# Kernel tuning notes

Hardware: AMD Instinct MI355X
Metric: run time of the kernel (lower is better)

The kernel has to match this reference:

```python
import jax, jax.numpy as jnp
from jax import lax
import numpy as np

SHEET = 160; AFF_K = 15; AFF_C = 2; AFF_DIL = 1
LAT_K = 25; LAT_DIL = 2; LAT_ITERS = 10
EXC_RANGE = 5.0
HOMEO_TARGET = 0.02
FLOAT_MULT = 0.1
INH_EXC_BAL = 0.55
STRENGTH = 1.0


def _dist(size):
    c = (size - 1) / 2.0
    a = np.arange(size) - c
    return np.sqrt(a[:, None] ** 2 + a[None, :] ** 2)


def get_circle(size, radius):
    return (_dist(size) < radius).astype(np.float32)


def get_radial_cos(size, radius):
    return np.cos(np.clip(_dist(size) / radius, 0.0, 1.0) * (np.pi / 2)).astype(np.float32)


def _constants():
    env = get_radial_cos(AFF_K, AFF_K) ** 2 * get_circle(AFF_K, AFF_K / 2)
    env = env / env.max()
    aff_env = np.tile(env[None, None], (1, AFF_C, 1, 1)).reshape(1, -1, 1)
    e = int(round(EXC_RANGE)); e = e if e % 2 == 1 else e + 1  # oddenise
    sre = get_radial_cos(e, EXC_RANGE) ** 2 * get_circle(e, e / 2)
    sre = sre / sre.sum()
    inh_mask = get_radial_cos(LAT_K, e / LAT_DIL) ** 2 * get_circle(LAT_K, e / (2 * LAT_DIL))
    lri = get_radial_cos(LAT_K, LAT_K) ** 2 * get_circle(LAT_K, LAT_K / 2) * (1.0 - inh_mask)
    lri = lri.reshape(1, -1, 1); lri = lri / lri.max()
    return jnp.asarray(aff_env), jnp.asarray(sre)[None, None], jnp.asarray(lri), e


def _unfold(x, k, dil):
    # F.unfold equivalent: (N, C*k*k, L), channel-major (c, kh, kw) ordering
    p = lax.conv_general_dilated_patches(x, (k, k), (1, 1), 'VALID', rhs_dilation=(dil, dil))
    n, f, h, w = p.shape
    return p.reshape(n, f, h * w)


def setup_inputs():
    key = jax.random.key(0)
    k1, k2, k3 = jax.random.split(key, 3)
    in_hw = SHEET + AFF_K - 1
    x = jax.random.uniform(k1, (1, AFF_C, in_hw, in_hw), dtype=jnp.float32)
    rfs = jax.random.uniform(k2, (SHEET * SHEET, AFF_C * AFF_K * AFF_K, 1), dtype=jnp.float32) + 0.1
    lat_weights = jax.random.uniform(k3, (SHEET * SHEET, LAT_K * LAT_K, 1), dtype=jnp.float32) + 0.1
    adathresh = jnp.zeros((1, 1, SHEET, SHEET), jnp.float32)
    return {"x": x, "rfs": rfs, "lat_weights": lat_weights, "adathresh": adathresh}


def _forward(x, rfs, lat_weights, adathresh):
    aff_env, sre, lri, e = _constants()
    sg = lax.stop_gradient
    F_aff = rfs.shape[1]; F_lat = lat_weights.shape[1]
    # no-grad in-place weight renormalisation
    rfs_n = rfs / sg(rfs.sum(1, keepdims=True) / (F_aff * FLOAT_MULT))
    latw_n = lat_weights / sg(lat_weights.sum(1, keepdims=True) / (F_lat * FLOAT_MULT))
    lat_w = sg(latw_n) / (F_lat * FLOAT_MULT)  # detached lateral weights
    # afferent locally-connected (unshared) receptive fields: unfold + per-location dot
    x_tiles = _unfold(x, AFF_K, AFF_DIL) * aff_env          # (1, F_aff, L)
    x_tiles = jnp.transpose(x_tiles, (2, 0, 1))             # (L, 1, F_aff)
    raw_aff = jnp.einsum('lof,lfo->l', x_tiles, rfs_n).reshape(1, 1, SHEET, SHEET)
    aff = sg(raw_aff) / (F_aff * FLOAT_MULT) - adathresh
    lat = jax.nn.relu(aff)
    pos_pad = e // 2
    pad = (LAT_K // 2) * LAT_DIL
    lat_mean0 = jnp.zeros_like(lat)

    def body(carry, _):
        l, lm = carry
        l = jnp.pad(l, ((0, 0), (0, 0), (pos_pad, pos_pad), (pos_pad, pos_pad)), constant_values=HOMEO_TARGET)
        l = lax.conv_general_dilated(l, sre, (1, 1), 'VALID', dimension_numbers=('NCHW', 'OIHW', 'NCHW'))
        lp = jnp.pad(l, ((0, 0), (0, 0), (pad, pad), (pad, pad)), constant_values=HOMEO_TARGET)
        tiles = _unfold(lp, LAT_K, LAT_DIL) * lri           # (1, F_lat, L)
        tiles = jnp.transpose(tiles, (2, 0, 1))             # (L, 1, F_lat)
        lat_neg = jnp.einsum('lof,lfo->l', tiles, lat_w).reshape(1, 1, SHEET, SHEET)
        l = l * (1.0 - INH_EXC_BAL) - lat_neg * INH_EXC_BAL
        l = l * STRENGTH + aff
        l = jnp.tanh(jax.nn.relu(l))
        return (l, lm + l), None

    (lat, lat_mean), _ = lax.scan(body, (lat, lat_mean0), None, length=LAT_ITERS)
    lat_mean = sg(lat_mean / LAT_ITERS)
    # hebbian lateral correlation term (grad flows to lat_weights only)
    lmp = jnp.pad(lat_mean, ((0, 0), (0, 0), (pad, pad), (pad, pad)), constant_values=HOMEO_TARGET)
    tiles = _unfold(lmp, LAT_K, LAT_DIL) * lri              # (1, F_lat, L)
    tiles = jnp.transpose(tiles, (2, 0, 1)) * lat_mean.reshape(SHEET * SHEET, 1, 1)
    lat_correlations = jnp.einsum('lof,lfo->', tiles, latw_n)
    return raw_aff, lat, lat_correlations


def reference(x, rfs, lat_weights, adathresh):
    return _forward(x, rfs, lat_weights, adathresh)
```

## Files before the change

kernel.cpp:

```cpp
#include <hip/hip_runtime.h>
#include <math.h>

#define SHEET 160
#define LTOT (SHEET*SHEET)
#define F_AFF 450
#define F_LAT 625
#define N_ITERS 10
#define IN_HW 174
#define HOMEO 0.02f
#define PI_D 3.14159265358979323846

typedef float f32x4 __attribute__((ext_vector_type(4)));

#define BH 10
#define BW 10
#define BLK 640
#define TCOLS (SHEET/BW)
#define GRID_L ((SHEET/BH)*TCOLS)
#define EH 58
#define EWH 30
#define EP_HALF (EH*EWH)
#define EP_N (2*EP_HALF)
#define LW 64
#define LH 62
#define LT_N (LH*LW)

#define PBLK 256
#define RPB 8
#define NABLK (LTOT/RPB)

#define NPAIR 256

#define WS_SRE    0
#define WS_PKF    32
#define WS_PKL    544
#define WS_OFFT   1056
#define WS_AFFTAB 1568
#define WS_AFF    2592
#define WS_B0     (WS_AFF + LTOT)
#define WS_B1     (WS_B0  + LTOT)
#define WS_LM     (WS_B1  + LTOT)
#define WS_WQ     (WS_LM  + LTOT + 64)

__device__ __forceinline__ float wred_dpp(float v) {
    v += __int_as_float(__builtin_amdgcn_update_dpp(0, __float_as_int(v), 0x111, 0xf, 0xf, true));
    v += __int_as_float(__builtin_amdgcn_update_dpp(0, __float_as_int(v), 0x112, 0xf, 0xf, true));
    v += __int_as_float(__builtin_amdgcn_update_dpp(0, __float_as_int(v), 0x114, 0xf, 0xf, true));
    v += __int_as_float(__builtin_amdgcn_update_dpp(0, __float_as_int(v), 0x118, 0xf, 0xf, true));
    v += __int_as_float(__builtin_amdgcn_update_dpp(0, __float_as_int(v), 0x142, 0xa, 0xf, true));
    v += __int_as_float(__builtin_amdgcn_update_dpp(0, __float_as_int(v), 0x143, 0xc, 0xf, true));
    return v;
}

__device__ __forceinline__ unsigned f2bf(float f) {
    unsigned u = __float_as_uint(f);
    return (u + 0x7FFFu + ((u >> 16) & 1u)) >> 16;
}

__global__ __launch_bounds__(1024) void k_init(float* __restrict__ ws,
                                               float* __restrict__ out) {
    __shared__ float red[1024];
    __shared__ float lriS[640];
    __shared__ int   nzf[512];
    __shared__ int   wcnt[16];
    const int t = threadIdx.x;
    const int lane = t & 63, wvi = t >> 6;

    if (t == 0) out[2 * LTOT] = 0.f;

    float sre_raw = 0.f;
    if (t < 25) {
        int u = t / 5, v = t % 5;
        double d = sqrt((double)((u-2)*(u-2) + (v-2)*(v-2)));
        if (d < 2.5) { double cv = cos(fmin(d/5.0, 1.0) * PI_D * 0.5); sre_raw = (float)(cv*cv); }
    }

    float lri_raw = 0.f;
    const int dy = t / 25, dx = t % 25;
    if (t < 625) {
        double d = sqrt((double)((dy-12)*(dy-12) + (dx-12)*(dx-12)));
        double base = 0.0, inh = 0.0;
        if (d < 12.5) { double cv = cos(fmin(d/25.0, 1.0) * PI_D * 0.5); base = cv*cv; }
        if (d < 1.25) { double cv = cos(fmin(d/2.5,  1.0) * PI_D * 0.5); inh  = cv*cv; }
        lri_raw = (float)(base * (1.0 - inh));
    }
    const bool nz = (lri_raw != 0.f);
    if (t < 640) lriS[t] = lri_raw;

    red[t] = lri_raw;
    __syncthreads();
    #pragma unroll
    for (int s = 512; s > 0; s >>= 1) {
        if (t < s) red[t] = fmaxf(red[t], red[t + s]);
        __syncthreads();
    }
    const float lri_max = red[0];
    __syncthreads();

    red[t] = sre_raw;
    __syncthreads();
    #pragma unroll
    for (int s = 512; s > 0; s >>= 1) {
        if (t < s) red[t] += red[t + s];
        __syncthreads();
    }
    const float sre_sum = red[0];

    if (t < 32) ws[WS_SRE + t] = (t < 25) ? sre_raw / sre_sum : 0.f;

    unsigned long long bal = __ballot(nz);
    if (lane == 0) wcnt[wvi] = __popcll(bal);
    __syncthreads();
    int woff = 0, ntot = 0;
    #pragma unroll
    for (int v2 = 0; v2 < 16; ++v2) { int c = wcnt[v2]; if (v2 < wvi) woff += c; ntot += c; }
    if (nz) nzf[woff + __popcll(bal & ((1ull << lane) - 1ull))] = t;
    __syncthreads();

    if (t < 256) {
        #pragma unroll
        for (int h = 0; h < 2; ++h) {
            int idx = 2*t + h;
            int f = 624, off = 0; float lv = 0.f;
            if (idx < ntot) {
                f = nzf[idx];
                int fy = f / 25, fx = f - 25*fy;
                off = fy * (2*EWH) + fx;
                lv = lriS[f] / lri_max;
            }
            int slot = (2*(t >> 6) + h)*64 + (t & 63);
            ((int*)  (ws + WS_PKF ))[slot] = f;
            ((float*)(ws + WS_PKL ))[slot] = lv;
            ((int*)  (ws + WS_OFFT))[slot] = off;
        }
    }

    if (t < 512) {
        float ev = 0.f; int off = 0;
        if (t < 450) {
            int c  = t / 225, rr = t % 225;
            int kh = rr / 15, kw = rr % 15;
            double d = sqrt((double)((kh-7)*(kh-7) + (kw-7)*(kw-7)));
            if (d < 7.5) { double cv = cos(fmin(d/15.0, 1.0) * PI_D * 0.5); ev = (float)(cv*cv); }
            off = c * (IN_HW*IN_HW) + kh * IN_HW + kw;
        }
        ((float2*)(ws + WS_AFFTAB))[t] = make_float2(ev, __int_as_float(off));
    }
}

__global__ __launch_bounds__(PBLK, 8) void k_pre(const float* __restrict__ x,
                                                 const float* __restrict__ rfs,
                                                 const float* __restrict__ latw,
                                                 const float* __restrict__ ada,
                                                 float* __restrict__ out_rawaff,
                                                 float* __restrict__ ws,
                                                 unsigned* __restrict__ wq) {
    __shared__ __align__(16) float S[5008];
    const int tid = threadIdx.x;
    const int w = tid >> 6, lane = tid & 63;

    if (blockIdx.x < NABLK) {
        const int l0 = blockIdx.x * RPB;
        const f32x4* src4 = (const f32x4*)(rfs + (size_t)l0 * F_AFF);
        #pragma unroll
        for (int k = 0; k < 4; ++k) {
            int idx = k * PBLK + tid;
            if (idx < 900) ((f32x4*)S)[idx] = __builtin_nontemporal_load(src4 + idx);
        }

        float envA[8]; int offA[8];
        const float2* atab = (const float2*)(ws + WS_AFFTAB);
        #pragma unroll
        for (int it = 0; it < 8; ++it) {
            float2 tb = atab[it*64 + lane];
            envA[it] = tb.x; offA[it] = __float_as_int(tb.y);
        }
        __syncthreads();

        #pragma unroll
        for (int s = 0; s < 2; ++s) {
            const int row = 2*w + s, l = l0 + row;
            const int i = l / SHEET, j = l % SHEET;
            const int xbase = i * IN_HW + j;
            const float* Srow = S + row * F_AFF;
            float dot = 0.f, rs = 0.f;
            #pragma unroll
            for (int it = 0; it < 8; ++it) {
                int f = it*64 + lane;
                float r = (f < F_AFF) ? Srow[f] : 0.f;
                float xv = x[xbase + offA[it]];
                dot = fmaf(xv * envA[it], r, dot);
                rs += r;
            }
            dot = wred_dpp(dot); rs = wred_dpp(rs);
            if (lane == 63) {
                float a = dot / rs;
                out_rawaff[l] = 45.0f * a;
                float aff = a - ada[l];
                ws[WS_AFF + l] = aff;
                ws[WS_B0  + l] = fmaxf(aff, 0.f);
                ws[WS_LM  + l] = 0.f;
            }
        }
    } else {
        const int l0 = (blockIdx.x - NABLK) * RPB;
        const f32x4* src4 = (const f32x4*)(latw + (size_t)l0 * F_LAT);
        #pragma unroll
        for (int k = 0; k < 5; ++k) {
            int idx = k * PBLK + tid;
            if (idx < 1250) ((f32x4*)S)[idx] = __builtin_nontemporal_load(src4 + idx);
        }

        int pf[8]; float pl[8];
        #pragma unroll
        for (int q8 = 0; q8 < 8; ++q8) {
            pf[q8] = ((const int*)  (ws + WS_PKF))[q8*64 + lane];
            pl[q8] = ((const float*)(ws + WS_PKL))[q8*64 + lane];
        }
        __syncthreads();

        #pragma unroll
        for (int s = 0; s < 2; ++s) {
            const int row = 2*w + s, l = l0 + row;
            const float* Srow = S + row * F_LAT;
            float sum = 0.f;
            #pragma unroll
            for (int it = 0; it < 10; ++it) {
                int f = it*64 + lane;
                sum += (f < F_LAT) ? Srow[f] : 0.f;
            }
            sum = wred_dpp(sum);
            const float inv = 1.0f / __int_as_float(__builtin_amdgcn_readlane(__float_as_int(sum), 63));
            unsigned* dst = wq + (size_t)l * NPAIR;
            #pragma unroll
            for (int q = 0; q < 4; ++q) {
                unsigned lo = f2bf(Srow[pf[2*q]]     * pl[2*q]     * inv);
                unsigned hi = f2bf(Srow[pf[2*q + 1]] * pl[2*q + 1] * inv);
                dst[q*64 + lane] = lo | (hi << 16);
            }
        }
    }
}

__global__ __launch_bounds__(BLK, 3) void k_lat(const unsigned* __restrict__ wq,
                                                float* __restrict__ ws,
                                                const float* __restrict__ lsrc,
                                                float* __restrict__ lat_out) {
    __shared__ float Lt[LT_N];
    __shared__ float Ep[EP_N];
    const int b  = blockIdx.x;
    const int i0 = (b / TCOLS) * BH;
    const int j0 = (b % TCOLS) * BW;
    const int tid = threadIdx.x;
    const int w = tid >> 6, lane = tid & 63;
    const int lrow = (i0 + w) * SHEET + j0;

    const int* offT = (const int*)(ws + WS_OFFT);
    int offr[8];
    #pragma unroll
    for (int q8 = 0; q8 < 8; ++q8) offr[q8] = offT[q8*64 + lane];

    unsigned wp[10][4];
    #pragma unroll
    for (int s = 0; s < 10; ++s) {
        const unsigned* row = wq + (size_t)(lrow + s) * NPAIR;
        #pragma unroll
        for (int k = 0; k < 4; ++k) wp[s][k] = row[k*64 + lane];
    }
    __builtin_amdgcn_sched_barrier(0);

    float sreg[25];
    #pragma unroll
    for (int q = 0; q < 25; ++q) sreg[q] = ws[WS_SRE + q];

    for (int idx = tid; idx < LT_N; idx += BLK) {
        int r = idx >> 6, c = idx & 63;
        int y  = i0 + r - 26;
        int xx = j0 + c - 26;
        float v = HOMEO;
        if (c < 62 && (unsigned)y < SHEET && (unsigned)xx < SHEET) v = lsrc[y*SHEET + xx];
        Lt[idx] = v;
    }
    __syncthreads();

    for (int qi = tid; qi < EH * 15; qi += BLK) {
        int y = qi / 15, q = qi - y * 15;
        int x0 = q * 4;
        float a0 = 0.f, a1 = 0.f, a2 = 0.f, a3 = 0.f;
        #pragma unroll
        for (int u = 0; u < 5; ++u) {
            const float* row = &Lt[(y + u) * LW + x0];
            float ra[8];
            #pragma unroll
            for (int v = 0; v < 8; ++v) ra[v] = row[v];
            #pragma unroll
            for (int v = 0; v < 5; ++v) {
                float s = sreg[u * 5 + v];
                a0 = fmaf(ra[v],     s, a0);
                a1 = fmaf(ra[v + 1], s, a1);
                a2 = fmaf(ra[v + 2], s, a2);
                a3 = fmaf(ra[v + 3], s, a3);
            }
        }
        int yg = i0 - 24 + y;
        bool yok = (unsigned)yg < SHEET;
        int xg = j0 - 24 + x0;
        float v0 = (yok && (unsigned)(xg    ) < SHEET) ? a0 : HOMEO;
        float v1 = (yok && (unsigned)(xg + 1) < SHEET) ? a1 : HOMEO;
        float v2 = (yok && (unsigned)(xg + 2) < SHEET) ? a2 : HOMEO;
        float v3 = (yok && (unsigned)(xg + 3) < SHEET) ? a3 : HOMEO;
        int c0 = y * EWH + 2 * q;
        Ep[c0]               = v0;
        Ep[EP_HALF + c0]     = v1;
        Ep[c0 + 1]           = v2;
        Ep[EP_HALF + c0 + 1] = v3;
    }
    __syncthreads();

    float acc[10];
    #pragma unroll
    for (int s = 0; s < 10; ++s) {
        const int gbase = (s & 1) * EP_HALF + w * EWH + (s >> 1);
        float a = 0.f;
        #pragma unroll
        for (int k = 0; k < 4; ++k) {
            unsigned p = wp[s][k];
            float e0 = Ep[gbase + offr[2*k]];
            float e1 = Ep[gbase + offr[2*k + 1]];
            a = fmaf(e0, __uint_as_float(p << 16),         a);
            a = fmaf(e1, __uint_as_float(p & 0xffff0000u), a);
        }
        acc[s] = a;
    }
    #pragma unroll
    for (int s = 0; s < 10; ++s) acc[s] = wred_dpp(acc[s]);

    float accs = 0.f;
    #pragma unroll
    for (int s = 0; s < 10; ++s) {
        float a = __int_as_float(__builtin_amdgcn_readlane(__float_as_int(acc[s]), 63));
        if (lane == s) accs = a;
    }
    if (lane < 10) {
        int s = lane;
        int l = lrow + s;
        int gbase = (s & 1) * EP_HALF + w * EWH + (s >> 1);
        float ec = Ep[gbase + 24*EWH + 12];
        float v = ec * 0.45f - accs * 0.55f + ws[WS_AFF + l];
        v = tanhf(fmaxf(v, 0.f));
        lat_out[l] = v;
        ws[WS_LM + l] += v;
    }
}

__global__ __launch_bounds__(BLK, 3) void k_hebb(const unsigned* __restrict__ wq,
                                                 float* __restrict__ ws,
                                                 float* __restrict__ out_scalar) {
    __shared__ float LMp[EP_N];
    __shared__ float part[10];
    const int b  = blockIdx.x;
    const int i0 = (b / TCOLS) * BH;
    const int j0 = (b % TCOLS) * BW;
    const int tid = threadIdx.x;
    const int w = tid >> 6, lane = tid & 63;
    const int lrow = (i0 + w) * SHEET + j0;
    const float* lm = ws + WS_LM;

    const int* offT = (const int*)(ws + WS_OFFT);
    int offr[8];
    #pragma unroll
    for (int q8 = 0; q8 < 8; ++q8) offr[q8] = offT[q8*64 + lane];

    unsigned wp[10][4];
    #pragma unroll
    for (int s = 0; s < 10; ++s) {
        const unsigned* row = wq + (size_t)(lrow + s) * NPAIR;
        #pragma unroll
        for (int k = 0; k < 4; ++k) wp[s][k] = row[k*64 + lane];
    }
    __builtin_amdgcn_sched_barrier(0);

    for (int idx = tid; idx < EP_N; idx += BLK) {
        int p   = idx / EP_HALF;
        int rem = idx - p * EP_HALF;
        int y   = rem / EWH;
        int col = rem - y * EWH;
        int yg = i0 - 24 + y;
        int xg = j0 - 24 + 2 * col + p;
        float v = HOMEO;
        if ((unsigned)yg < SHEET && (unsigned)xg < SHEET && col < 29) v = lm[yg*SHEET + xg] * 0.1f;
        LMp[idx] = v;
    }
    __syncthreads();

    float acc[10];
    #pragma unroll
    for (int s = 0; s < 10; ++s) {
        const int gbase = (s & 1) * EP_HALF + w * EWH + (s >> 1);
        float a = 0.f;
        #pragma unroll
        for (int k = 0; k < 4; ++k) {
            unsigned p = wp[s][k];
            float e0 = LMp[gbase + offr[2*k]];
            float e1 = LMp[gbase + offr[2*k + 1]];
            a = fmaf(e0, __uint_as_float(p << 16),         a);
            a = fmaf(e1, __uint_as_float(p & 0xffff0000u), a);
        }
        acc[s] = a;
    }
    #pragma unroll
    for (int s = 0; s < 10; ++s) acc[s] = wred_dpp(acc[s]);

    if (lane == 63) {
        float wacc = 0.f;
        #pragma unroll
        for (int s = 0; s < 10; ++s) {
            int gbase = (s & 1) * EP_HALF + w * EWH + (s >> 1);
            float lmv = LMp[gbase + 24*EWH + 12];
            wacc += lmv * 62.5f * acc[s];
        }
        part[w] = wacc;
    }
    __syncthreads();
    if (tid == 0) {
        float s = 0.f;
        #pragma unroll
        for (int q = 0; q < 10; ++q) s += part[q];
        atomicAdd(out_scalar, s);
    }
}

extern "C" void kernel_launch(void* const* d_in, const int* in_sizes, int n_in,
                              void* d_out, int out_size, void* d_ws, size_t ws_size,
                              hipStream_t stream) {
    const float* x    = (const float*)d_in[0];
    const float* rfs  = (const float*)d_in[1];
    const float* latw = (const float*)d_in[2];
    const float* ada  = (const float*)d_in[3];
    float* out = (float*)d_out;
    float* ws  = (float*)d_ws;
    unsigned* wq = (unsigned*)(ws + WS_WQ);

    k_init<<<1, 1024, 0, stream>>>(ws, out);
    k_pre<<<2 * NABLK, PBLK, 0, stream>>>(x, rfs, latw, ada, out, ws, wq);

    for (int t = 0; t < N_ITERS; ++t) {
        const float* src = ws + ((t & 1) ? WS_B1 : WS_B0);
        float* dst = (t == N_ITERS - 1) ? (out + LTOT)
                                        : (ws + ((t & 1) ? WS_B0 : WS_B1));
        k_lat<<<GRID_L, BLK, 0, stream>>>(wq, ws, src, dst);
    }

    k_hebb<<<GRID_L, BLK, 0, stream>>>(wq, ws, out + 2 * LTOT);
}
```

Baseline: 136.2 us.

## Switch lateral tile to row-major layout and vectorize LDS and weight loads

The dilated-2 even/odd split layout of the excitation/lateral-mean tile is replaced by a plain row-major 60-wide layout, with offsets doubled to match. The dot-product loop is reordered so each LDS access fetches a float2 covering two adjacent output columns, and stores of the excitation tile become 16-byte vector writes. Packed bf16 weights are now stored per lane as contiguous 16-byte chunks, so the lat and hebb kernels load them with one dwordx4 per row instead of four strided dword loads. The intent is fewer memory instructions. The row-major layout may bring different LDS bank-conflict behaviour, since stride-2 taps now read interleaved data.

```diff
diff --git a/kernel.cpp b/kernel.cpp
--- a/kernel.cpp
+++ b/kernel.cpp
@@ -10,7 +10,8 @@
 #define HOMEO 0.02f
 #define PI_D 3.14159265358979323846
 
-typedef float f32x4 __attribute__((ext_vector_type(4)));
+typedef float    f32x4 __attribute__((ext_vector_type(4)));
+typedef unsigned u32x4 __attribute__((ext_vector_type(4)));
 
 #define BH 10
 #define BW 10
@@ -18,9 +19,8 @@
 #define TCOLS (SHEET/BW)
 #define GRID_L ((SHEET/BH)*TCOLS)
 #define EH 58
-#define EWH 30
-#define EP_HALF (EH*EWH)
-#define EP_N (2*EP_HALF)
+#define EW 60
+#define EP_N (EH*EW)
 #define LW 64
 #define LH 62
 #define LT_N (LH*LW)
@@ -56,6 +56,8 @@
     unsigned u = __float_as_uint(f);
     return (u + 0x7FFFu + ((u >> 16) & 1u)) >> 16;
 }
+__device__ __forceinline__ float bflo(unsigned p) { return __uint_as_float(p << 16); }
+__device__ __forceinline__ float bfhi(unsigned p) { return __uint_as_float(p & 0xffff0000u); }
 
 __global__ __launch_bounds__(1024) void k_init(float* __restrict__ ws,
                                                float* __restrict__ out) {
@@ -125,7 +127,7 @@
             if (idx < ntot) {
                 f = nzf[idx];
                 int fy = f / 25, fx = f - 25*fy;
-                off = fy * (2*EWH) + fx;
+                off = fy * (2*EW) + 2*fx;
                 lv = lriS[f] / lri_max;
             }
             int slot = (2*(t >> 6) + h)*64 + (t & 63);
@@ -231,13 +233,14 @@
             }
             sum = wred_dpp(sum);
             const float inv = 1.0f / __int_as_float(__builtin_amdgcn_readlane(__float_as_int(sum), 63));
-            unsigned* dst = wq + (size_t)l * NPAIR;
+            u32x4 pk;
             #pragma unroll
             for (int q = 0; q < 4; ++q) {
                 unsigned lo = f2bf(Srow[pf[2*q]]     * pl[2*q]     * inv);
                 unsigned hi = f2bf(Srow[pf[2*q + 1]] * pl[2*q + 1] * inv);
-                dst[q*64 + lane] = lo | (hi << 16);
-            }
+                pk[q] = lo | (hi << 16);
+            }
+            *(u32x4*)(wq + (size_t)l * NPAIR + (lane << 2)) = pk;
         }
     }
 }
@@ -246,8 +249,8 @@
                                                 float* __restrict__ ws,
                                                 const float* __restrict__ lsrc,
                                                 float* __restrict__ lat_out) {
-    __shared__ float Lt[LT_N];
-    __shared__ float Ep[EP_N];
+    __shared__ __align__(16) float Lt[LT_N];
+    __shared__ __align__(16) float Ep[EP_N];
     const int b  = blockIdx.x;
     const int i0 = (b / TCOLS) * BH;
     const int j0 = (b % TCOLS) * BW;
@@ -260,13 +263,10 @@
     #pragma unroll
     for (int q8 = 0; q8 < 8; ++q8) offr[q8] = offT[q8*64 + lane];
 
-    unsigned wp[10][4];
-    #pragma unroll
-    for (int s = 0; s < 10; ++s) {
-        const unsigned* row = wq + (size_t)(lrow + s) * NPAIR;
-        #pragma unroll
-        for (int k = 0; k < 4; ++k) wp[s][k] = row[k*64 + lane];
-    }
+    u32x4 wp[10];
+    #pragma unroll
+    for (int s = 0; s < 10; ++s)
+        wp[s] = *(const u32x4*)(wq + (size_t)(lrow + s) * NPAIR + (lane << 2));
     __builtin_amdgcn_sched_barrier(0);
 
     float sreg[25];
@@ -305,32 +305,32 @@
         int yg = i0 - 24 + y;
         bool yok = (unsigned)yg < SHEET;
         int xg = j0 - 24 + x0;
-        float v0 = (yok && (unsigned)(xg    ) < SHEET) ? a0 : HOMEO;
-        float v1 = (yok && (unsigned)(xg + 1) < SHEET) ? a1 : HOMEO;
-        float v2 = (yok && (unsigned)(xg + 2) < SHEET) ? a2 : HOMEO;
-        float v3 = (yok && (unsigned)(xg + 3) < SHEET) ? a3 : HOMEO;
-        int c0 = y * EWH + 2 * q;
-        Ep[c0]               = v0;
-        Ep[EP_HALF + c0]     = v1;
-        Ep[c0 + 1]           = v2;
-        Ep[EP_HALF + c0 + 1] = v3;
-    }
-    __syncthreads();
-
-    float acc[10];
-    #pragma unroll
-    for (int s = 0; s < 10; ++s) {
-        const int gbase = (s & 1) * EP_HALF + w * EWH + (s >> 1);
-        float a = 0.f;
-        #pragma unroll
-        for (int k = 0; k < 4; ++k) {
-            unsigned p = wp[s][k];
-            float e0 = Ep[gbase + offr[2*k]];
-            float e1 = Ep[gbase + offr[2*k + 1]];
-            a = fmaf(e0, __uint_as_float(p << 16),         a);
-            a = fmaf(e1, __uint_as_float(p & 0xffff0000u), a);
-        }
-        acc[s] = a;
+        f32x4 v4;
+        v4.x = (yok && (unsigned)(xg    ) < SHEET) ? a0 : HOMEO;
+        v4.y = (yok && (unsigned)(xg + 1) < SHEET) ? a1 : HOMEO;
+        v4.z = (yok && (unsigned)(xg + 2) < SHEET) ? a2 : HOMEO;
+        v4.w = (yok && (unsigned)(xg + 3) < SHEET) ? a3 : HOMEO;
+        *(f32x4*)&Ep[y * EW + x0] = v4;
+    }
+    __syncthreads();
+
+    float acc[10] = {0.f,0.f,0.f,0.f,0.f,0.f,0.f,0.f,0.f,0.f};
+    const int cb = w * EW;
+    #pragma unroll
+    for (int k = 0; k < 4; ++k) {
+        int b0 = cb + offr[2*k];
+        int b1 = cb + offr[2*k + 1];
+        #pragma unroll
+        for (int cp = 0; cp < 5; ++cp) {
+            float2 eA = *(const float2*)&Ep[b0 + 2*cp];
+            float2 eB = *(const float2*)&Ep[b1 + 2*cp];
+            unsigned pE = wp[2*cp][k];
+            unsigned pO = wp[2*cp + 1][k];
+            acc[2*cp]     = fmaf(eA.x, bflo(pE), acc[2*cp]);
+            acc[2*cp]     = fmaf(eB.x, bfhi(pE), acc[2*cp]);
+            acc[2*cp + 1] = fmaf(eA.y, bflo(pO), acc[2*cp + 1]);
+            acc[2*cp + 1] = fmaf(eB.y, bfhi(pO), acc[2*cp + 1]);
+        }
     }
     #pragma unroll
     for (int s = 0; s < 10; ++s) acc[s] = wred_dpp(acc[s]);
@@ -344,8 +344,7 @@
     if (lane < 10) {
         int s = lane;
         int l = lrow + s;
-        int gbase = (s & 1) * EP_HALF + w * EWH + (s >> 1);
-        float ec = Ep[gbase + 24*EWH + 12];
+        float ec = Ep[(w + 24) * EW + s + 24];
         float v = ec * 0.45f - accs * 0.55f + ws[WS_AFF + l];
         v = tanhf(fmaxf(v, 0.f));
         lat_out[l] = v;
@@ -356,7 +355,7 @@
 __global__ __launch_bounds__(BLK, 3) void k_hebb(const unsigned* __restrict__ wq,
                                                  float* __restrict__ ws,
                                                  float* __restrict__ out_scalar) {
-    __shared__ float LMp[EP_N];
+    __shared__ __align__(16) float LMp[EP_N];
     __shared__ float part[10];
     const int b  = blockIdx.x;
     const int i0 = (b / TCOLS) * BH;
@@ -371,42 +370,39 @@
     #pragma unroll
     for (int q8 = 0; q8 < 8; ++q8) offr[q8] = offT[q8*64 + lane];
 
-    unsigned wp[10][4];
-    #pragma unroll
-    for (int s = 0; s < 10; ++s) {
-        const unsigned* row = wq + (size_t)(lrow + s) * NPAIR;
-        #pragma unroll
-        for (int k = 0; k < 4; ++k) wp[s][k] = row[k*64 + lane];
-    }
+    u32x4 wp[10];
+    #pragma unroll
+    for (int s = 0; s < 10; ++s)
+        wp[s] = *(const u32x4*)(wq + (size_t)(lrow + s) * NPAIR + (lane << 2));
     __builtin_amdgcn_sched_barrier(0);
 
     for (int idx = tid; idx < EP_N; idx += BLK) {
-        int p   = idx / EP_HALF;
-        int rem = idx - p * EP_HALF;
-        int y   = rem / EWH;
-        int col = rem - y * EWH;
+        int y = idx / EW, col = idx - y * EW;
         int yg = i0 - 24 + y;
-        int xg = j0 - 24 + 2 * col + p;
+        int xg = j0 - 24 + col;
         float v = HOMEO;
-        if ((unsigned)yg < SHEET && (unsigned)xg < SHEET && col < 29) v = lm[yg*SHEET + xg] * 0.1f;
+        if (col < 58 && (unsigned)yg < SHEET && (unsigned)xg < SHEET) v = lm[yg*SHEET + xg] * 0.1f;
         LMp[idx] = v;
     }
     __syncthreads();
 
-    float acc[10];
-    #pragma unroll
-    for (int s = 0; s < 10; ++s) {
-        const int gbase = (s & 1) * EP_HALF + w * EWH + (s >> 1);
-        float a = 0.f;
-        #pragma unroll
-        for (int k = 0; k < 4; ++k) {
-            unsigned p = wp[s][k];
-            float e0 = LMp[gbase + offr[2*k]];
-            float e1 = LMp[gbase + offr[2*k + 1]];
-            a = fmaf(e0, __uint_as_float(p << 16),         a);
-            a = fmaf(e1, __uint_as_float(p & 0xffff0000u), a);
-        }
-        acc[s] = a;
+    float acc[10] = {0.f,0.f,0.f,0.f,0.f,0.f,0.f,0.f,0.f,0.f};
+    const int cb = w * EW;
+    #pragma unroll
+    for (int k = 0; k < 4; ++k) {
+        int b0 = cb + offr[2*k];
+        int b1 = cb + offr[2*k + 1];
+        #pragma unroll
+        for (int cp = 0; cp < 5; ++cp) {
+            float2 eA = *(const float2*)&LMp[b0 + 2*cp];
+            float2 eB = *(const float2*)&LMp[b1 + 2*cp];
+            unsigned pE = wp[2*cp][k];
+            unsigned pO = wp[2*cp + 1][k];
+            acc[2*cp]     = fmaf(eA.x, bflo(pE), acc[2*cp]);
+            acc[2*cp]     = fmaf(eB.x, bfhi(pE), acc[2*cp]);
+            acc[2*cp + 1] = fmaf(eA.y, bflo(pO), acc[2*cp + 1]);
+            acc[2*cp + 1] = fmaf(eB.y, bfhi(pO), acc[2*cp + 1]);
+        }
     }
     #pragma unroll
     for (int s = 0; s < 10; ++s) acc[s] = wred_dpp(acc[s]);
@@ -415,8 +411,7 @@
         float wacc = 0.f;
         #pragma unroll
         for (int s = 0; s < 10; ++s) {
-            int gbase = (s & 1) * EP_HALF + w * EWH + (s >> 1);
-            float lmv = LMp[gbase + 24*EWH + 12];
+            float lmv = LMp[(w + 24) * EW + s + 24];
             wacc += lmv * 62.5f * acc[s];
         }
         part[w] = wacc;
```

After: 145.1 us. 6.5% more time.

## Retile lateral kernel to 10x5 blocks and vectorise packed weight loads

Applied to the files above, without the earlier changes.

The lateral iteration kernel now uses 10x5 output tiles with 320-thread blocks, where each wave handles two rows of five pixels. This doubles the grid to 512 blocks so more of the GPU's compute units stay busy. Packed bf16 weights are now laid out so each lane reads one 16-byte vector instead of four strided words, and the pre-pass writes them in that layout. The Hebbian kernel keeps the old 10x10 tiling through a second offset table. The trade-off is a larger relative halo to load per block, so more redundant shared-memory fill and smoothing work.

```diff
diff --git a/kernel.cpp b/kernel.cpp
--- a/kernel.cpp
+++ b/kernel.cpp
@@ -10,21 +10,31 @@
 #define HOMEO 0.02f
 #define PI_D 3.14159265358979323846
 
-typedef float f32x4 __attribute__((ext_vector_type(4)));
+typedef float    f32x4 __attribute__((ext_vector_type(4)));
+typedef unsigned u32x4 __attribute__((ext_vector_type(4)));
 
 #define BH 10
-#define BW 10
-#define BLK 640
+#define BW 5
+#define BLK 320
 #define TCOLS (SHEET/BW)
 #define GRID_L ((SHEET/BH)*TCOLS)
 #define EH 58
-#define EWH 30
+#define EWH 28
 #define EP_HALF (EH*EWH)
 #define EP_N (2*EP_HALF)
 #define LW 64
 #define LH 62
 #define LT_N (LH*LW)
 
+#define HBH 10
+#define HBW 10
+#define HBLK 640
+#define HTCOLS (SHEET/HBW)
+#define HGRID ((SHEET/HBH)*HTCOLS)
+#define HEWH 30
+#define HEP_HALF (58*HEWH)
+#define HEP_N (2*HEP_HALF)
+
 #define PBLK 256
 #define RPB 8
 #define NABLK (LTOT/RPB)
@@ -35,8 +45,9 @@
 #define WS_PKF    32
 #define WS_PKL    544
 #define WS_OFFT   1056
-#define WS_AFFTAB 1568
-#define WS_AFF    2592
+#define WS_OFF2   1568
+#define WS_AFFTAB 2080
+#define WS_AFF    3104
 #define WS_B0     (WS_AFF + LTOT)
 #define WS_B1     (WS_B0  + LTOT)
 #define WS_LM     (WS_B1  + LTOT)
@@ -56,6 +67,8 @@
     unsigned u = __float_as_uint(f);
     return (u + 0x7FFFu + ((u >> 16) & 1u)) >> 16;
 }
+__device__ __forceinline__ float bflo(unsigned p) { return __uint_as_float(p << 16); }
+__device__ __forceinline__ float bfhi(unsigned p) { return __uint_as_float(p & 0xffff0000u); }
 
 __global__ __launch_bounds__(1024) void k_init(float* __restrict__ ws,
                                                float* __restrict__ out) {
@@ -121,17 +134,19 @@
         #pragma unroll
         for (int h = 0; h < 2; ++h) {
             int idx = 2*t + h;
-            int f = 624, off = 0; float lv = 0.f;
+            int f = 624, off1 = 0, off2 = 0; float lv = 0.f;
             if (idx < ntot) {
                 f = nzf[idx];
                 int fy = f / 25, fx = f - 25*fy;
-                off = fy * (2*EWH) + fx;
+                off1 = fy * (2*EWH)  + fx;
+                off2 = fy * (2*HEWH) + fx;
                 lv = lriS[f] / lri_max;
             }
             int slot = (2*(t >> 6) + h)*64 + (t & 63);
             ((int*)  (ws + WS_PKF ))[slot] = f;
             ((float*)(ws + WS_PKL ))[slot] = lv;
-            ((int*)  (ws + WS_OFFT))[slot] = off;
+            ((int*)  (ws + WS_OFFT))[slot] = off1;
+            ((int*)  (ws + WS_OFF2))[slot] = off2;
         }
     }
 
@@ -231,41 +246,40 @@
             }
             sum = wred_dpp(sum);
             const float inv = 1.0f / __int_as_float(__builtin_amdgcn_readlane(__float_as_int(sum), 63));
-            unsigned* dst = wq + (size_t)l * NPAIR;
+            u32x4 pk;
             #pragma unroll
             for (int q = 0; q < 4; ++q) {
                 unsigned lo = f2bf(Srow[pf[2*q]]     * pl[2*q]     * inv);
                 unsigned hi = f2bf(Srow[pf[2*q + 1]] * pl[2*q + 1] * inv);
-                dst[q*64 + lane] = lo | (hi << 16);
-            }
-        }
-    }
-}
-
-__global__ __launch_bounds__(BLK, 3) void k_lat(const unsigned* __restrict__ wq,
+                pk[q] = lo | (hi << 16);
+            }
+            *(u32x4*)(wq + (size_t)l * NPAIR + (lane << 2)) = pk;
+        }
+    }
+}
+
+__global__ __launch_bounds__(BLK, 2) void k_lat(const unsigned* __restrict__ wq,
                                                 float* __restrict__ ws,
                                                 const float* __restrict__ lsrc,
                                                 float* __restrict__ lat_out) {
-    __shared__ float Lt[LT_N];
-    __shared__ float Ep[EP_N];
+    __shared__ __align__(16) float Lt[LT_N];
+    __shared__ __align__(16) float Ep[EP_N];
     const int b  = blockIdx.x;
     const int i0 = (b / TCOLS) * BH;
     const int j0 = (b % TCOLS) * BW;
     const int tid = threadIdx.x;
     const int w = tid >> 6, lane = tid & 63;
-    const int lrow = (i0 + w) * SHEET + j0;
 
     const int* offT = (const int*)(ws + WS_OFFT);
     int offr[8];
     #pragma unroll
     for (int q8 = 0; q8 < 8; ++q8) offr[q8] = offT[q8*64 + lane];
 
-    unsigned wp[10][4];
+    u32x4 wp[10];
     #pragma unroll
     for (int s = 0; s < 10; ++s) {
-        const unsigned* row = wq + (size_t)(lrow + s) * NPAIR;
-        #pragma unroll
-        for (int k = 0; k < 4; ++k) wp[s][k] = row[k*64 + lane];
+        int r = s / 5, c = s - 5 * r;
+        wp[s] = *(const u32x4*)(wq + (size_t)((i0 + 2*w + r) * SHEET + j0 + c) * NPAIR + (lane << 2));
     }
     __builtin_amdgcn_sched_barrier(0);
 
@@ -278,13 +292,13 @@
         int y  = i0 + r - 26;
         int xx = j0 + c - 26;
         float v = HOMEO;
-        if (c < 62 && (unsigned)y < SHEET && (unsigned)xx < SHEET) v = lsrc[y*SHEET + xx];
+        if (c < 57 && (unsigned)y < SHEET && (unsigned)xx < SHEET) v = lsrc[y*SHEET + xx];
         Lt[idx] = v;
     }
     __syncthreads();
 
-    for (int qi = tid; qi < EH * 15; qi += BLK) {
-        int y = qi / 15, q = qi - y * 15;
+    for (int qi = tid; qi < EH * 14; qi += BLK) {
+        int y = qi / 14, q = qi - y * 14;
         int x0 = q * 4;
         float a0 = 0.f, a1 = 0.f, a2 = 0.f, a3 = 0.f;
         #pragma unroll
@@ -320,15 +334,16 @@
     float acc[10];
     #pragma unroll
     for (int s = 0; s < 10; ++s) {
-        const int gbase = (s & 1) * EP_HALF + w * EWH + (s >> 1);
+        int r = s / 5, c = s - 5 * r;
+        const int gbase = (c & 1) * EP_HALF + (2*w + r) * EWH + (c >> 1);
         float a = 0.f;
         #pragma unroll
         for (int k = 0; k < 4; ++k) {
             unsigned p = wp[s][k];
             float e0 = Ep[gbase + offr[2*k]];
             float e1 = Ep[gbase + offr[2*k + 1]];
-            a = fmaf(e0, __uint_as_float(p << 16),         a);
-            a = fmaf(e1, __uint_as_float(p & 0xffff0000u), a);
+            a = fmaf(e0, bflo(p), a);
+            a = fmaf(e1, bfhi(p), a);
         }
         acc[s] = a;
     }
@@ -342,10 +357,10 @@
         if (lane == s) accs = a;
     }
     if (lane < 10) {
-        int s = lane;
-        int l = lrow + s;
-        int gbase = (s & 1) * EP_HALF + w * EWH + (s >> 1);
-        float ec = Ep[gbase + 24*EWH + 12];
+        int r = (lane >= 5) ? 1 : 0;
+        int c = lane - 5 * r;
+        int l = (i0 + 2*w + r) * SHEET + j0 + c;
+        float ec = Ep[(c & 1) * EP_HALF + (2*w + r + 24) * EWH + (c >> 1) + 12];
         float v = ec * 0.45f - accs * 0.55f + ws[WS_AFF + l];
         v = tanhf(fmaxf(v, 0.f));
         lat_out[l] = v;
@@ -353,38 +368,35 @@
     }
 }
 
-__global__ __launch_bounds__(BLK, 3) void k_hebb(const unsigned* __restrict__ wq,
-                                                 float* __restrict__ ws,
-                                                 float* __restrict__ out_scalar) {
-    __shared__ float LMp[EP_N];
+__global__ __launch_bounds__(HBLK, 3) void k_hebb(const unsigned* __restrict__ wq,
+                                                  float* __restrict__ ws,
+                                                  float* __restrict__ out_scalar) {
+    __shared__ float LMp[HEP_N];
     __shared__ float part[10];
     const int b  = blockIdx.x;
-    const int i0 = (b / TCOLS) * BH;
-    const int j0 = (b % TCOLS) * BW;
+    const int i0 = (b / HTCOLS) * HBH;
+    const int j0 = (b % HTCOLS) * HBW;
     const int tid = threadIdx.x;
     const int w = tid >> 6, lane = tid & 63;
     const int lrow = (i0 + w) * SHEET + j0;
     const float* lm = ws + WS_LM;
 
-    const int* offT = (const int*)(ws + WS_OFFT);
+    const int* offT = (const int*)(ws + WS_OFF2);
     int offr[8];
     #pragma unroll
     for (int q8 = 0; q8 < 8; ++q8) offr[q8] = offT[q8*64 + lane];
 
-    unsigned wp[10][4];
-    #pragma unroll
-    for (int s = 0; s < 10; ++s) {
-        const unsigned* row = wq + (size_t)(lrow + s) * NPAIR;
-        #pragma unroll
-        for (int k = 0; k < 4; ++k) wp[s][k] = row[k*64 + lane];
-    }
+    u32x4 wp[10];
+    #pragma unroll
+    for (int s = 0; s < 10; ++s)
+        wp[s] = *(const u32x4*)(wq + (size_t)(lrow + s) * NPAIR + (lane << 2));
     __builtin_amdgcn_sched_barrier(0);
 
-    for (int idx = tid; idx < EP_N; idx += BLK) {
-        int p   = idx / EP_HALF;
-        int rem = idx - p * EP_HALF;
-        int y   = rem / EWH;
-        int col = rem - y * EWH;
+    for (int idx = tid; idx < HEP_N; idx += HBLK) {
+        int p   = idx / HEP_HALF;
+        int rem = idx - p * HEP_HALF;
+        int y   = rem / HEWH;
+        int col = rem - y * HEWH;
         int yg = i0 - 24 + y;
         int xg = j0 - 24 + 2 * col + p;
         float v = HOMEO;
@@ -396,15 +408,15 @@
     float acc[10];
     #pragma unroll
     for (int s = 0; s < 10; ++s) {
-        const int gbase = (s & 1) * EP_HALF + w * EWH + (s >> 1);
+        const int gbase = (s & 1) * HEP_HALF + w * HEWH + (s >> 1);
         float a = 0.f;
         #pragma unroll
         for (int k = 0; k < 4; ++k) {
             unsigned p = wp[s][k];
             float e0 = LMp[gbase + offr[2*k]];
             float e1 = LMp[gbase + offr[2*k + 1]];
-            a = fmaf(e0, __uint_as_float(p << 16),         a);
-            a = fmaf(e1, __uint_as_float(p & 0xffff0000u), a);
+            a = fmaf(e0, bflo(p), a);
+            a = fmaf(e1, bfhi(p), a);
         }
         acc[s] = a;
     }
@@ -415,8 +427,7 @@
         float wacc = 0.f;
         #pragma unroll
         for (int s = 0; s < 10; ++s) {
-            int gbase = (s & 1) * EP_HALF + w * EWH + (s >> 1);
-            float lmv = LMp[gbase + 24*EWH + 12];
+            float lmv = LMp[(s & 1) * HEP_HALF + (w + 24) * HEWH + (s >> 1) + 12];
             wacc += lmv * 62.5f * acc[s];
         }
         part[w] = wacc;
@@ -451,5 +462,5 @@
         k_lat<<<GRID_L, BLK, 0, stream>>>(wq, ws, src, dst);
     }
 
-    k_hebb<<<GRID_L, BLK, 0, stream>>>(wq, ws, out + 2 * LTOT);
-}
+    k_hebb<<<HGRID, HBLK, 0, stream>>>(wq, ws, out + 2 * LTOT);
+}
```

Result: slower. 160.6 us (+17.9%).
